# Performance work log

Measured on AMD Instinct MI355X. Metric: run time of the kernel, lower is better.

Reference implementation:

```python
import jax, jax.numpy as jnp
import numpy as np

B, C, H, W = 4, 256, 64, 64
C8 = C // 8


def setup_inputs() -> dict:
    key = jax.random.key(0)
    ks = jax.random.split(key, 9)
    s_in = 1.0 / np.sqrt(C)
    return {
        "x": jax.random.normal(ks[0], (B, C, H, W), dtype=jnp.float32),
        "Wq": jax.random.normal(ks[1], (C8, C), dtype=jnp.float32) * s_in,
        "bq": jax.random.normal(ks[2], (C8,), dtype=jnp.float32) * 0.01,
        "Wk": jax.random.normal(ks[3], (C8, C), dtype=jnp.float32) * s_in,
        "bk": jax.random.normal(ks[4], (C8,), dtype=jnp.float32) * 0.01,
        "Wv": jax.random.normal(ks[5], (C, C), dtype=jnp.float32) * s_in,
        "bv": jax.random.normal(ks[6], (C,), dtype=jnp.float32) * 0.01,
        "Wo": jax.random.normal(ks[7], (C, C), dtype=jnp.float32) * s_in,
        "bo": jax.random.normal(ks[8], (C,), dtype=jnp.float32) * 0.01,
    }


def reference(x, Wq, bq, Wk, bk, Wv, bv, Wo, bo):
    b, c, h, w = x.shape
    n = h * w
    xf = x.reshape(b, c, n)                                   # (B, C, N)
    # 1x1 convs are channel GEMMs
    q = jnp.einsum('bcn,dc->bnd', xf, Wq) + bq                # (B, N, C8)
    k = jnp.einsum('bcn,dc->bdn', xf, Wk) + bk[:, None]       # (B, C8, N)
    v = jnp.einsum('bcn,dc->bdn', xf, Wv) + bv[:, None]       # (B, C, N)
    energy = jnp.einsum('bnd,bdm->bnm', q, k)                 # (B, N, N)
    attn = jax.nn.softmax(energy, axis=-1)
    # out[b,c,i] = sum_j v[b,c,j] * attn[b,i,j]
    out = jnp.einsum('bcj,bij->bci', v, attn)                 # (B, C, N)
    out = out.reshape(b, c, h, w) + x                         # residual
    out = jnp.einsum('bchw,dc->bdhw', out, Wo) + bo[None, :, None, None]
    return out
```

## Files before the change

### kernel.cpp

```cpp
#include <hip/hip_runtime.h>

#define DEV __device__ __forceinline__

constexpr int B_  = 4;
constexpr int C_  = 256;
constexpr int C8_ = 32;
constexpr int N_  = 4096;

using u16 = unsigned short;
using u32 = unsigned int;

typedef __attribute__((ext_vector_type(8))) short bf16x8;
typedef __attribute__((ext_vector_type(4))) float f32x4;

DEV float bf2f(u16 u) { return __uint_as_float(((u32)u) << 16); }
DEV u16   f2bf(float f) {
  u32 i = __float_as_uint(f);
  i += 0x7fffu + ((i >> 16) & 1u);
  return (u16)(i >> 16);
}

DEV void cvt8(const float* p, bf16x8& hi, bf16x8& lo) {
  float4 a = *(const float4*)p;
  float4 b = *(const float4*)(p + 4);
  float f[8] = {a.x, a.y, a.z, a.w, b.x, b.y, b.z, b.w};
  #pragma unroll
  for (int j = 0; j < 8; ++j) {
    u16 h = f2bf(f[j]);
    hi[j] = (short)h;
    lo[j] = (short)f2bf(f[j] - bf2f(h));
  }
}

__global__ __launch_bounds__(256) void qkv_mfma(
    const float* __restrict__ x,
    const float* __restrict__ Wq, const float* __restrict__ bq,
    const float* __restrict__ Wk, const float* __restrict__ bk,
    const float* __restrict__ Wv, const float* __restrict__ bv,
    u16* __restrict__ qt, u16* __restrict__ kt, u16* __restrict__ vb,
    u16* __restrict__ xT)
{
  __shared__ __align__(16) u16 xh[64][264];
  __shared__ __align__(16) u16 xl[64][264];

  const int tid  = threadIdx.x;
  const int lane = tid & 63;
  const int w    = tid >> 6;
  const int m    = lane & 15;
  const int quad = lane >> 4;
  const int b    = blockIdx.y;
  const int n0   = blockIdx.x * 64;

  {
    const int nl = tid & 63, cb = tid >> 6;
    #pragma unroll 4
    for (int cc = 0; cc < 64; ++cc) {
      int c = cb + cc * 4;
      float v = x[((size_t)b * C_ + c) * N_ + n0 + nl];
      u16 h = f2bf(v);
      xh[nl][c] = h;
      xl[nl][c] = f2bf(v - bf2f(h));
    }
  }
  __syncthreads();

  #pragma unroll
  for (int it = 0; it < 8; ++it) {
    int idx = tid + it * 256;
    int n = idx >> 5, q = idx & 31;
    *(uint4*)&xT[((size_t)b * N_ + n0 + n) * C_ + q * 8] = *(const uint4*)&xh[n][q * 8];
  }

  f32x4 ov[4][4];
  f32x4 oq[4];
  #pragma unroll
  for (int dt = 0; dt < 4; ++dt)
    #pragma unroll
    for (int nt = 0; nt < 4; ++nt) ov[dt][nt] = (f32x4){0.f, 0.f, 0.f, 0.f};
  #pragma unroll
  for (int nt = 0; nt < 4; ++nt) oq[nt] = (f32x4){0.f, 0.f, 0.f, 0.f};

  const float* Wqk = (w < 2) ? (Wq + (size_t)(w * 16) * C_)
                             : (Wk + (size_t)((w - 2) * 16) * C_);

  for (int K = 0; K < 8; ++K) {
    bf16x8 xfh[4], xfl[4];
    #pragma unroll
    for (int nt = 0; nt < 4; ++nt) {
      xfh[nt] = *(const bf16x8*)&xh[nt * 16 + m][K * 32 + quad * 8];
      xfl[nt] = *(const bf16x8*)&xl[nt * 16 + m][K * 32 + quad * 8];
    }
    #pragma unroll
    for (int dt = 0; dt < 4; ++dt) {
      bf16x8 whi, wlo;
      cvt8(Wv + (size_t)(64 * w + dt * 16 + m) * C_ + K * 32 + quad * 8, whi, wlo);
      #pragma unroll
      for (int nt = 0; nt < 4; ++nt) {
        ov[dt][nt] = __builtin_amdgcn_mfma_f32_16x16x32_bf16(whi, xfh[nt], ov[dt][nt], 0, 0, 0);
        ov[dt][nt] = __builtin_amdgcn_mfma_f32_16x16x32_bf16(whi, xfl[nt], ov[dt][nt], 0, 0, 0);
        ov[dt][nt] = __builtin_amdgcn_mfma_f32_16x16x32_bf16(wlo, xfh[nt], ov[dt][nt], 0, 0, 0);
      }
    }
    {
      bf16x8 bhi, blo;
      cvt8(Wqk + (size_t)m * C_ + K * 32 + quad * 8, bhi, blo);
      #pragma unroll
      for (int nt = 0; nt < 4; ++nt) {
        oq[nt] = __builtin_amdgcn_mfma_f32_16x16x32_bf16(xfh[nt], bhi, oq[nt], 0, 0, 0);
        oq[nt] = __builtin_amdgcn_mfma_f32_16x16x32_bf16(xfl[nt], bhi, oq[nt], 0, 0, 0);
        oq[nt] = __builtin_amdgcn_mfma_f32_16x16x32_bf16(xfh[nt], blo, oq[nt], 0, 0, 0);
      }
    }
  }

  #pragma unroll
  for (int dt = 0; dt < 4; ++dt) {
    #pragma unroll
    for (int r = 0; r < 4; ++r) {
      int oc = 64 * w + dt * 16 + quad * 4 + r;
      float bias = bv[oc];
      #pragma unroll
      for (int nt = 0; nt < 4; ++nt)
        vb[((size_t)b * C_ + oc) * N_ + n0 + nt * 16 + m] = f2bf(ov[dt][nt][r] + bias);
    }
  }
  {
    u16* qk_out = (w < 2) ? qt : kt;
    const float* qk_bias = (w < 2) ? bq : bk;
    int dbase = (w & 1) * 16;
    float bias = qk_bias[dbase + m];
    #pragma unroll
    for (int nt = 0; nt < 4; ++nt)
      #pragma unroll
      for (int r = 0; r < 4; ++r)
        qk_out[((size_t)b * N_ + n0 + nt * 16 + quad * 4 + r) * C8_ + dbase + m] =
            f2bf(oq[nt][r] + bias);
  }
}

__global__ __launch_bounds__(256) void attn_mfma(
    const u16* __restrict__ qt,
    const u16* __restrict__ kt,
    const u16* __restrict__ vb,
    float* __restrict__ Opart,
    float* __restrict__ ml)
{
  __shared__ __align__(16) u16  ps[2][64][136];
  __shared__ __align__(16) float als[2][64];

  const int tid  = threadIdx.x;
  const int lane = tid & 63;
  const int w    = tid >> 6;
  const int m    = lane & 15;
  const int quad = lane >> 4;

  const int lid = blockIdx.x + gridDim.x * (blockIdx.y + gridDim.y * blockIdx.z);
  const int grp = lid & 7;
  const int ksl = grp & 1;
  const int b   = grp >> 1;
  const int i0  = (lid >> 3) * 64;

  const bf16x8 qfrag =
      *(const bf16x8*)(qt + ((size_t)b * N_ + i0 + w * 16 + m) * C8_ + quad * 8);

  const u16* kbase = kt + (size_t)b * N_ * C8_;
  const u16* vrow  = vb + ((size_t)b * C_ + w * 64 + m) * N_;

  f32x4 o[4][4];
  #pragma unroll
  for (int t = 0; t < 4; ++t)
    #pragma unroll
    for (int ct = 0; ct < 4; ++ct) o[t][ct] = (f32x4){0.f, 0.f, 0.f, 0.f};
  float m_r = -1e30f, l_r = 0.f;

  const int jbeg = ksl * 2048, jend = jbeg + 2048;
  int buf = 0;

  for (int j0 = jbeg; j0 < jend; j0 += 128, buf ^= 1) {
    bf16x8 kA[8];
    #pragma unroll
    for (int t = 0; t < 8; ++t)
      kA[t] = *(const bf16x8*)(kbase + (size_t)(j0 + t * 16 + m) * C8_ + quad * 8);
    bf16x8 vB[4][4];
    #pragma unroll
    for (int ct = 0; ct < 4; ++ct)
      #pragma unroll
      for (int kk = 0; kk < 4; ++kk)
        vB[ct][kk] = *(const bf16x8*)(vrow + (size_t)ct * 16 * N_ + j0 + kk * 32 + quad * 8);

    f32x4 s[8];
    #pragma unroll
    for (int t = 0; t < 8; ++t)
      s[t] = __builtin_amdgcn_mfma_f32_16x16x32_bf16(
          kA[t], qfrag, (f32x4){0.f, 0.f, 0.f, 0.f}, 0, 0, 0);

    float mx = -1e30f;
    #pragma unroll
    for (int t = 0; t < 8; ++t)
      #pragma unroll
      for (int r = 0; r < 4; ++r) mx = fmaxf(mx, s[t][r]);
    mx = fmaxf(mx, __shfl_xor(mx, 16));
    mx = fmaxf(mx, __shfl_xor(mx, 32));
    float mn = fmaxf(m_r, mx);
    float al = __expf(m_r - mn);
    m_r = mn;
    float p[8][4], sm = 0.f;
    #pragma unroll
    for (int t = 0; t < 8; ++t)
      #pragma unroll
      for (int r = 0; r < 4; ++r) {
        p[t][r] = __expf(s[t][r] - mn);
        sm += p[t][r];
      }
    sm += __shfl_xor(sm, 16);
    sm += __shfl_xor(sm, 32);
    l_r = l_r * al + sm;

    #pragma unroll
    for (int t = 0; t < 8; ++t) {
      u32 lo = (u32)f2bf(p[t][0]) | ((u32)f2bf(p[t][1]) << 16);
      u32 hi = (u32)f2bf(p[t][2]) | ((u32)f2bf(p[t][3]) << 16);
      *(uint2*)&ps[buf][w * 16 + m][t * 16 + quad * 4] = make_uint2(lo, hi);
    }
    if (quad == 0) als[buf][w * 16 + m] = al;

    __syncthreads();

    #pragma unroll
    for (int t = 0; t < 4; ++t) {
      float4 alv = *(const float4*)&als[buf][t * 16 + quad * 4];
      #pragma unroll
      for (int ct = 0; ct < 4; ++ct) {
        o[t][ct][0] *= alv.x; o[t][ct][1] *= alv.y;
        o[t][ct][2] *= alv.z; o[t][ct][3] *= alv.w;
      }
    }

    #pragma unroll
    for (int t = 0; t < 4; ++t) {
      #pragma unroll
      for (int kk = 0; kk < 4; ++kk) {
        bf16x8 pf = *(const bf16x8*)&ps[buf][t * 16 + m][kk * 32 + quad * 8];
        #pragma unroll
        for (int ct = 0; ct < 4; ++ct)
          o[t][ct] = __builtin_amdgcn_mfma_f32_16x16x32_bf16(pf, vB[ct][kk], o[t][ct], 0, 0, 0);
      }
    }
  }

  float* Ob = Opart + (size_t)ksl * B_ * N_ * C_ + ((size_t)b * N_ + i0) * C_ + w * 64;
  #pragma unroll
  for (int t = 0; t < 4; ++t)
    #pragma unroll
    for (int ct = 0; ct < 4; ++ct)
      #pragma unroll
      for (int r = 0; r < 4; ++r)
        Ob[(size_t)(t * 16 + quad * 4 + r) * C_ + ct * 16 + m] = o[t][ct][r];

  if (quad == 0) {
    size_t mli = ((size_t)ksl * B_ + b) * N_ + i0 + w * 16 + m;
    ml[mli] = m_r;
    ml[(size_t)2 * B_ * N_ + mli] = l_r;
  }
}

__global__ __launch_bounds__(256) void combine(
    const float* __restrict__ Opart, const float* __restrict__ ml,
    u16* __restrict__ hb)
{
  __shared__ __align__(16) u16 st[64][264];
  const int tid = threadIdx.x;
  const int b   = blockIdx.y;
  const int n0  = blockIdx.x * 64;
  const int nl  = tid & 63;
  const int cg  = tid >> 6;

  size_t base = (size_t)b * N_ + n0 + nl;
  float m0 = ml[base];
  float m1 = ml[(size_t)B_ * N_ + base];
  float l0 = ml[(size_t)2 * B_ * N_ + base];
  float l1 = ml[(size_t)3 * B_ * N_ + base];
  float M  = fmaxf(m0, m1);
  float w0 = __expf(m0 - M), w1 = __expf(m1 - M);
  float inv = 1.f / (l0 * w0 + l1 * w1);
  w0 *= inv; w1 *= inv;

  const float* O0 = Opart + base * C_ + cg * 64;
  const float* O1 = O0 + (size_t)B_ * N_ * C_;
  #pragma unroll
  for (int cc = 0; cc < 64; cc += 4) {
    float4 a  = *(const float4*)(O0 + cc);
    float4 c2 = *(const float4*)(O1 + cc);
    u32 lo = (u32)f2bf(a.x * w0 + c2.x * w1) | ((u32)f2bf(a.y * w0 + c2.y * w1) << 16);
    u32 hi = (u32)f2bf(a.z * w0 + c2.z * w1) | ((u32)f2bf(a.w * w0 + c2.w * w1) << 16);
    *(uint2*)&st[nl][cg * 64 + cc] = make_uint2(lo, hi);
  }
  __syncthreads();

  #pragma unroll
  for (int it = 0; it < 8; ++it) {
    int idx = tid + it * 256;
    int n = idx >> 5, q = idx & 31;
    *(uint4*)&hb[((size_t)b * N_ + n0 + n) * C_ + q * 8] = *(const uint4*)&st[n][q * 8];
  }
}

__global__ __launch_bounds__(256) void out_mfma(
    const u16* __restrict__ hb, const u16* __restrict__ xT,
    const float* __restrict__ Wo, const float* __restrict__ bo,
    float* __restrict__ out)
{
  const int tid  = threadIdx.x;
  const int lane = tid & 63;
  const int w    = tid >> 6;
  const int m    = lane & 15;
  const int quad = lane >> 4;
  const int b    = blockIdx.y;
  const int n0   = blockIdx.x * 64;

  f32x4 o[4][4];
  #pragma unroll
  for (int dt = 0; dt < 4; ++dt)
    #pragma unroll
    for (int nt = 0; nt < 4; ++nt) o[dt][nt] = (f32x4){0.f, 0.f, 0.f, 0.f};

  for (int K = 0; K < 8; ++K) {
    bf16x8 hf[4], xf[4];
    #pragma unroll
    for (int nt = 0; nt < 4; ++nt) {
      size_t row = (size_t)b * N_ + n0 + nt * 16 + m;
      hf[nt] = *(const bf16x8*)(hb + row * C_ + K * 32 + quad * 8);
      xf[nt] = *(const bf16x8*)(xT + row * C_ + K * 32 + quad * 8);
    }
    #pragma unroll
    for (int dt = 0; dt < 4; ++dt) {
      bf16x8 whi, wlo;
      cvt8(Wo + (size_t)(64 * w + dt * 16 + m) * C_ + K * 32 + quad * 8, whi, wlo);
      #pragma unroll
      for (int nt = 0; nt < 4; ++nt) {
        o[dt][nt] = __builtin_amdgcn_mfma_f32_16x16x32_bf16(whi, hf[nt], o[dt][nt], 0, 0, 0);
        o[dt][nt] = __builtin_amdgcn_mfma_f32_16x16x32_bf16(wlo, hf[nt], o[dt][nt], 0, 0, 0);
        o[dt][nt] = __builtin_amdgcn_mfma_f32_16x16x32_bf16(whi, xf[nt], o[dt][nt], 0, 0, 0);
        o[dt][nt] = __builtin_amdgcn_mfma_f32_16x16x32_bf16(wlo, xf[nt], o[dt][nt], 0, 0, 0);
      }
    }
  }

  #pragma unroll
  for (int dt = 0; dt < 4; ++dt)
    #pragma unroll
    for (int r = 0; r < 4; ++r) {
      int d = 64 * w + dt * 16 + quad * 4 + r;
      float bias = bo[d];
      #pragma unroll
      for (int nt = 0; nt < 4; ++nt)
        out[((size_t)b * C_ + d) * N_ + n0 + nt * 16 + m] = o[dt][nt][r] + bias;
    }
}

extern "C" void kernel_launch(void* const* d_in, const int* in_sizes, int n_in,
                              void* d_out, int out_size, void* d_ws, size_t ws_size,
                              hipStream_t stream)
{
  const float* x  = (const float*)d_in[0];
  const float* Wq = (const float*)d_in[1];
  const float* bq = (const float*)d_in[2];
  const float* Wk = (const float*)d_in[3];
  const float* bk = (const float*)d_in[4];
  const float* Wv = (const float*)d_in[5];
  const float* bv = (const float*)d_in[6];
  const float* Wo = (const float*)d_in[7];
  const float* bo = (const float*)d_in[8];

  u16* qt = (u16*)d_ws;
  u16* kt = qt + (size_t)B_ * N_ * C8_;
  u16* vb = kt + (size_t)B_ * N_ * C8_;
  u16* hb = vb + (size_t)B_ * C_ * N_;
  u16* xT = hb + (size_t)B_ * C_ * N_;
  float* Opart = (float*)(xT + (size_t)B_ * N_ * C_);
  float* ml = Opart + (size_t)2 * B_ * N_ * C_;

  float* out = (float*)d_out;

  qkv_mfma<<<dim3(N_ / 64, B_), 256, 0, stream>>>(
      x, Wq, bq, Wk, bk, Wv, bv, qt, kt, vb, xT);
  attn_mfma<<<dim3(N_ / 64, 2, B_), 256, 0, stream>>>(qt, kt, vb, Opart, ml);
  combine<<<dim3(N_ / 64, B_), 256, 0, stream>>>(Opart, ml, hb);
  out_mfma<<<dim3(N_ / 64, B_), 256, 0, stream>>>(hb, xT, Wo, bo, out);
}
```

Before: 228.7 us.

## Presplit weights, transpose x separately, prefetch K/V in attention, fuse combine into output GEMM

Adds a weight-split kernel that converts the weights to bf16 hi/lo pairs once, and an x-transpose kernel that writes hi/lo bf16 copies of x. The QKV and output GEMMs now read these directly with 32-wide tiles, which doubles the number of blocks. The attention kernel software-prefetches the next K and V fragments, keeps half of V resident, and skips rescaling when no row max changed. The separate combine kernel is folded into the output GEMM, which reads the fp32 partials directly. This removes redundant per-block conversion work and a launch, at the cost of extra kernels, more workspace traffic and higher register pressure.

```diff
diff --git a/kernel.cpp b/kernel.cpp
--- a/kernel.cpp
+++ b/kernel.cpp
@@ -20,117 +20,134 @@
   return (u16)(i >> 16);
 }
 
-DEV void cvt8(const float* p, bf16x8& hi, bf16x8& lo) {
-  float4 a = *(const float4*)p;
-  float4 b = *(const float4*)(p + 4);
-  float f[8] = {a.x, a.y, a.z, a.w, b.x, b.y, b.z, b.w};
-  #pragma unroll
-  for (int j = 0; j < 8; ++j) {
-    u16 h = f2bf(f[j]);
-    hi[j] = (short)h;
-    lo[j] = (short)f2bf(f[j] - bf2f(h));
+__global__ __launch_bounds__(256) void wsplit(
+    const float* __restrict__ Wq, const float* __restrict__ Wk,
+    const float* __restrict__ Wv, const float* __restrict__ Wo,
+    u16* __restrict__ WqH, u16* __restrict__ WqL,
+    u16* __restrict__ WkH, u16* __restrict__ WkL,
+    u16* __restrict__ WvH, u16* __restrict__ WvL,
+    u16* __restrict__ WoH, u16* __restrict__ WoL)
+{
+  int i = blockIdx.x * 256 + threadIdx.x;
+  const float* src; u16 *h, *l; int off;
+  if (i < 8192)        { src = Wq; h = WqH; l = WqL; off = i; }
+  else if (i < 16384)  { src = Wk; h = WkH; l = WkL; off = i - 8192; }
+  else if (i < 81920)  { src = Wv; h = WvH; l = WvL; off = i - 16384; }
+  else                 { src = Wo; h = WoH; l = WoL; off = i - 81920; }
+  float v = src[off];
+  u16 hi = f2bf(v);
+  h[off] = hi;
+  l[off] = f2bf(v - bf2f(hi));
+}
+
+__global__ __launch_bounds__(256) void xprep(
+    const float* __restrict__ x, u16* __restrict__ xTh, u16* __restrict__ xTl)
+{
+  __shared__ float tf[64][65];
+  const int tid = threadIdx.x;
+  const int b = blockIdx.z, c0 = blockIdx.y * 64, n0 = blockIdx.x * 64;
+  const int nl = tid & 63, cb = tid >> 6;
+
+  #pragma unroll
+  for (int cc = 0; cc < 16; ++cc) {
+    int cl = cb * 16 + cc;
+    tf[nl][cl] = x[((size_t)b * C_ + c0 + cl) * N_ + n0 + nl];
+  }
+  __syncthreads();
+
+  #pragma unroll
+  for (int it = 0; it < 2; ++it) {
+    int idx = tid + it * 256;
+    int n = idx >> 3, q = idx & 7;
+    u32 ph[4], pl[4];
+    #pragma unroll
+    for (int j = 0; j < 4; ++j) {
+      float v0 = tf[n][q * 8 + 2 * j], v1 = tf[n][q * 8 + 2 * j + 1];
+      u16 h0 = f2bf(v0), h1 = f2bf(v1);
+      ph[j] = (u32)h0 | ((u32)h1 << 16);
+      pl[j] = (u32)f2bf(v0 - bf2f(h0)) | ((u32)f2bf(v1 - bf2f(h1)) << 16);
+    }
+    size_t off = ((size_t)b * N_ + n0 + n) * C_ + c0 + q * 8;
+    *(uint4*)&xTh[off] = make_uint4(ph[0], ph[1], ph[2], ph[3]);
+    *(uint4*)&xTl[off] = make_uint4(pl[0], pl[1], pl[2], pl[3]);
   }
 }
 
 __global__ __launch_bounds__(256) void qkv_mfma(
-    const float* __restrict__ x,
-    const float* __restrict__ Wq, const float* __restrict__ bq,
-    const float* __restrict__ Wk, const float* __restrict__ bk,
-    const float* __restrict__ Wv, const float* __restrict__ bv,
-    u16* __restrict__ qt, u16* __restrict__ kt, u16* __restrict__ vb,
-    u16* __restrict__ xT)
-{
-  __shared__ __align__(16) u16 xh[64][264];
-  __shared__ __align__(16) u16 xl[64][264];
-
-  const int tid  = threadIdx.x;
-  const int lane = tid & 63;
-  const int w    = tid >> 6;
-  const int m    = lane & 15;
-  const int quad = lane >> 4;
-  const int b    = blockIdx.y;
-  const int n0   = blockIdx.x * 64;
-
-  {
-    const int nl = tid & 63, cb = tid >> 6;
-    #pragma unroll 4
-    for (int cc = 0; cc < 64; ++cc) {
-      int c = cb + cc * 4;
-      float v = x[((size_t)b * C_ + c) * N_ + n0 + nl];
-      u16 h = f2bf(v);
-      xh[nl][c] = h;
-      xl[nl][c] = f2bf(v - bf2f(h));
-    }
-  }
-  __syncthreads();
-
-  #pragma unroll
-  for (int it = 0; it < 8; ++it) {
-    int idx = tid + it * 256;
-    int n = idx >> 5, q = idx & 31;
-    *(uint4*)&xT[((size_t)b * N_ + n0 + n) * C_ + q * 8] = *(const uint4*)&xh[n][q * 8];
-  }
-
-  f32x4 ov[4][4];
-  f32x4 oq[4];
+    const u16* __restrict__ xTh, const u16* __restrict__ xTl,
+    const u16* __restrict__ WqH, const u16* __restrict__ WqL,
+    const u16* __restrict__ WkH, const u16* __restrict__ WkL,
+    const u16* __restrict__ WvH, const u16* __restrict__ WvL,
+    const float* __restrict__ bq, const float* __restrict__ bk,
+    const float* __restrict__ bv,
+    u16* __restrict__ qt, u16* __restrict__ kt, u16* __restrict__ vb)
+{
+  const int tid = threadIdx.x;
+  const int lane = tid & 63, w = tid >> 6, m = lane & 15, quad = lane >> 4;
+  const int b = blockIdx.y, n0 = blockIdx.x * 32;
+
+  const u16* qkH = (w < 2) ? (WqH + (size_t)(w * 16 + m) * C_)
+                           : (WkH + (size_t)((w - 2) * 16 + m) * C_);
+  const u16* qkL = (w < 2) ? (WqL + (size_t)(w * 16 + m) * C_)
+                           : (WkL + (size_t)((w - 2) * 16 + m) * C_);
+  const size_t nr0 = (size_t)b * N_ + n0 + m;
+
+  f32x4 ov[4][2], oq[2];
   #pragma unroll
   for (int dt = 0; dt < 4; ++dt)
     #pragma unroll
-    for (int nt = 0; nt < 4; ++nt) ov[dt][nt] = (f32x4){0.f, 0.f, 0.f, 0.f};
-  #pragma unroll
-  for (int nt = 0; nt < 4; ++nt) oq[nt] = (f32x4){0.f, 0.f, 0.f, 0.f};
-
-  const float* Wqk = (w < 2) ? (Wq + (size_t)(w * 16) * C_)
-                             : (Wk + (size_t)((w - 2) * 16) * C_);
+    for (int nt = 0; nt < 2; ++nt) ov[dt][nt] = (f32x4){0.f, 0.f, 0.f, 0.f};
+  #pragma unroll
+  for (int nt = 0; nt < 2; ++nt) oq[nt] = (f32x4){0.f, 0.f, 0.f, 0.f};
 
   for (int K = 0; K < 8; ++K) {
-    bf16x8 xfh[4], xfl[4];
-    #pragma unroll
-    for (int nt = 0; nt < 4; ++nt) {
-      xfh[nt] = *(const bf16x8*)&xh[nt * 16 + m][K * 32 + quad * 8];
-      xfl[nt] = *(const bf16x8*)&xl[nt * 16 + m][K * 32 + quad * 8];
+    const int ko = K * 32 + quad * 8;
+    bf16x8 xh[2], xl[2];
+    #pragma unroll
+    for (int nt = 0; nt < 2; ++nt) {
+      xh[nt] = *(const bf16x8*)(xTh + (nr0 + nt * 16) * C_ + ko);
+      xl[nt] = *(const bf16x8*)(xTl + (nr0 + nt * 16) * C_ + ko);
     }
     #pragma unroll
     for (int dt = 0; dt < 4; ++dt) {
-      bf16x8 whi, wlo;
-      cvt8(Wv + (size_t)(64 * w + dt * 16 + m) * C_ + K * 32 + quad * 8, whi, wlo);
-      #pragma unroll
-      for (int nt = 0; nt < 4; ++nt) {
-        ov[dt][nt] = __builtin_amdgcn_mfma_f32_16x16x32_bf16(whi, xfh[nt], ov[dt][nt], 0, 0, 0);
-        ov[dt][nt] = __builtin_amdgcn_mfma_f32_16x16x32_bf16(whi, xfl[nt], ov[dt][nt], 0, 0, 0);
-        ov[dt][nt] = __builtin_amdgcn_mfma_f32_16x16x32_bf16(wlo, xfh[nt], ov[dt][nt], 0, 0, 0);
+      bf16x8 whi = *(const bf16x8*)(WvH + (size_t)(64 * w + dt * 16 + m) * C_ + ko);
+      bf16x8 wlo = *(const bf16x8*)(WvL + (size_t)(64 * w + dt * 16 + m) * C_ + ko);
+      #pragma unroll
+      for (int nt = 0; nt < 2; ++nt) {
+        ov[dt][nt] = __builtin_amdgcn_mfma_f32_16x16x32_bf16(whi, xh[nt], ov[dt][nt], 0, 0, 0);
+        ov[dt][nt] = __builtin_amdgcn_mfma_f32_16x16x32_bf16(whi, xl[nt], ov[dt][nt], 0, 0, 0);
+        ov[dt][nt] = __builtin_amdgcn_mfma_f32_16x16x32_bf16(wlo, xh[nt], ov[dt][nt], 0, 0, 0);
       }
     }
     {
-      bf16x8 bhi, blo;
-      cvt8(Wqk + (size_t)m * C_ + K * 32 + quad * 8, bhi, blo);
-      #pragma unroll
-      for (int nt = 0; nt < 4; ++nt) {
-        oq[nt] = __builtin_amdgcn_mfma_f32_16x16x32_bf16(xfh[nt], bhi, oq[nt], 0, 0, 0);
-        oq[nt] = __builtin_amdgcn_mfma_f32_16x16x32_bf16(xfl[nt], bhi, oq[nt], 0, 0, 0);
-        oq[nt] = __builtin_amdgcn_mfma_f32_16x16x32_bf16(xfh[nt], blo, oq[nt], 0, 0, 0);
+      bf16x8 bhi = *(const bf16x8*)(qkH + ko);
+      bf16x8 blo = *(const bf16x8*)(qkL + ko);
+      #pragma unroll
+      for (int nt = 0; nt < 2; ++nt) {
+        oq[nt] = __builtin_amdgcn_mfma_f32_16x16x32_bf16(xh[nt], bhi, oq[nt], 0, 0, 0);
+        oq[nt] = __builtin_amdgcn_mfma_f32_16x16x32_bf16(xl[nt], bhi, oq[nt], 0, 0, 0);
+        oq[nt] = __builtin_amdgcn_mfma_f32_16x16x32_bf16(xh[nt], blo, oq[nt], 0, 0, 0);
       }
     }
   }
 
   #pragma unroll
-  for (int dt = 0; dt < 4; ++dt) {
+  for (int dt = 0; dt < 4; ++dt)
     #pragma unroll
     for (int r = 0; r < 4; ++r) {
       int oc = 64 * w + dt * 16 + quad * 4 + r;
       float bias = bv[oc];
       #pragma unroll
-      for (int nt = 0; nt < 4; ++nt)
+      for (int nt = 0; nt < 2; ++nt)
         vb[((size_t)b * C_ + oc) * N_ + n0 + nt * 16 + m] = f2bf(ov[dt][nt][r] + bias);
     }
-  }
   {
     u16* qk_out = (w < 2) ? qt : kt;
-    const float* qk_bias = (w < 2) ? bq : bk;
+    const float* qbias = (w < 2) ? bq : bk;
     int dbase = (w & 1) * 16;
-    float bias = qk_bias[dbase + m];
-    #pragma unroll
-    for (int nt = 0; nt < 4; ++nt)
+    float bias = qbias[dbase + m];
+    #pragma unroll
+    for (int nt = 0; nt < 2; ++nt)
       #pragma unroll
       for (int r = 0; r < 4; ++r)
         qk_out[((size_t)b * N_ + n0 + nt * 16 + quad * 4 + r) * C8_ + dbase + m] =
@@ -138,31 +155,23 @@
   }
 }
 
-__global__ __launch_bounds__(256) void attn_mfma(
-    const u16* __restrict__ qt,
-    const u16* __restrict__ kt,
+__global__ __launch_bounds__(256, 2) void attn_mfma(
+    const u16* __restrict__ qt, const u16* __restrict__ kt,
     const u16* __restrict__ vb,
-    float* __restrict__ Opart,
-    float* __restrict__ ml)
+    float* __restrict__ Opart, float* __restrict__ ml)
 {
   __shared__ __align__(16) u16  ps[2][64][136];
   __shared__ __align__(16) float als[2][64];
 
-  const int tid  = threadIdx.x;
-  const int lane = tid & 63;
-  const int w    = tid >> 6;
-  const int m    = lane & 15;
-  const int quad = lane >> 4;
+  const int tid = threadIdx.x, lane = tid & 63, w = tid >> 6;
+  const int m = lane & 15, quad = lane >> 4;
 
   const int lid = blockIdx.x + gridDim.x * (blockIdx.y + gridDim.y * blockIdx.z);
-  const int grp = lid & 7;
-  const int ksl = grp & 1;
-  const int b   = grp >> 1;
-  const int i0  = (lid >> 3) * 64;
+  const int grp = lid & 7, ksl = grp & 1, b = grp >> 1;
+  const int i0 = (lid >> 3) * 64;
 
   const bf16x8 qfrag =
       *(const bf16x8*)(qt + ((size_t)b * N_ + i0 + w * 16 + m) * C8_ + quad * 8);
-
   const u16* kbase = kt + (size_t)b * N_ * C8_;
   const u16* vrow  = vb + ((size_t)b * C_ + w * 64 + m) * N_;
 
@@ -176,17 +185,22 @@
   const int jbeg = ksl * 2048, jend = jbeg + 2048;
   int buf = 0;
 
+  bf16x8 kA[8], vB01[2][4], vB23[2][4];
+  #pragma unroll
+  for (int t = 0; t < 8; ++t)
+    kA[t] = *(const bf16x8*)(kbase + (size_t)(jbeg + t * 16 + m) * C8_ + quad * 8);
+  #pragma unroll
+  for (int ct = 0; ct < 2; ++ct)
+    #pragma unroll
+    for (int kk = 0; kk < 4; ++kk)
+      vB01[ct][kk] = *(const bf16x8*)(vrow + (size_t)ct * 16 * N_ + jbeg + kk * 32 + quad * 8);
+
   for (int j0 = jbeg; j0 < jend; j0 += 128, buf ^= 1) {
-    bf16x8 kA[8];
-    #pragma unroll
-    for (int t = 0; t < 8; ++t)
-      kA[t] = *(const bf16x8*)(kbase + (size_t)(j0 + t * 16 + m) * C8_ + quad * 8);
-    bf16x8 vB[4][4];
-    #pragma unroll
-    for (int ct = 0; ct < 4; ++ct)
+    #pragma unroll
+    for (int ct = 0; ct < 2; ++ct)
       #pragma unroll
       for (int kk = 0; kk < 4; ++kk)
-        vB[ct][kk] = *(const bf16x8*)(vrow + (size_t)ct * 16 * N_ + j0 + kk * 32 + quad * 8);
+        vB23[ct][kk] = *(const bf16x8*)(vrow + (size_t)(ct + 2) * 16 * N_ + j0 + kk * 32 + quad * 8);
 
     f32x4 s[8];
     #pragma unroll
@@ -226,14 +240,34 @@
 
     __syncthreads();
 
-    #pragma unroll
-    for (int t = 0; t < 4; ++t) {
-      float4 alv = *(const float4*)&als[buf][t * 16 + quad * 4];
-      #pragma unroll
-      for (int ct = 0; ct < 4; ++ct) {
-        o[t][ct][0] *= alv.x; o[t][ct][1] *= alv.y;
-        o[t][ct][2] *= alv.z; o[t][ct][3] *= alv.w;
-      }
+    const int jn = j0 + 128;
+    bf16x8 kAn[8], vBn[2][4];
+    if (jn < jend) {
+      #pragma unroll
+      for (int t = 0; t < 8; ++t)
+        kAn[t] = *(const bf16x8*)(kbase + (size_t)(jn + t * 16 + m) * C8_ + quad * 8);
+      #pragma unroll
+      for (int ct = 0; ct < 2; ++ct)
+        #pragma unroll
+        for (int kk = 0; kk < 4; ++kk)
+          vBn[ct][kk] = *(const bf16x8*)(vrow + (size_t)ct * 16 * N_ + jn + kk * 32 + quad * 8);
+    }
+
+    float4 alv[4];
+    #pragma unroll
+    for (int t = 0; t < 4; ++t) alv[t] = *(const float4*)&als[buf][t * 16 + quad * 4];
+    float am = 1.f;
+    #pragma unroll
+    for (int t = 0; t < 4; ++t)
+      am = fminf(am, fminf(fminf(alv[t].x, alv[t].y), fminf(alv[t].z, alv[t].w)));
+    if (__any(am < 1.f)) {
+      #pragma unroll
+      for (int t = 0; t < 4; ++t)
+        #pragma unroll
+        for (int ct = 0; ct < 4; ++ct) {
+          o[t][ct][0] *= alv[t].x; o[t][ct][1] *= alv[t].y;
+          o[t][ct][2] *= alv[t].z; o[t][ct][3] *= alv[t].w;
+        }
     }
 
     #pragma unroll
@@ -241,10 +275,20 @@
       #pragma unroll
       for (int kk = 0; kk < 4; ++kk) {
         bf16x8 pf = *(const bf16x8*)&ps[buf][t * 16 + m][kk * 32 + quad * 8];
+        o[t][0] = __builtin_amdgcn_mfma_f32_16x16x32_bf16(pf, vB01[0][kk], o[t][0], 0, 0, 0);
+        o[t][1] = __builtin_amdgcn_mfma_f32_16x16x32_bf16(pf, vB01[1][kk], o[t][1], 0, 0, 0);
+        o[t][2] = __builtin_amdgcn_mfma_f32_16x16x32_bf16(pf, vB23[0][kk], o[t][2], 0, 0, 0);
+        o[t][3] = __builtin_amdgcn_mfma_f32_16x16x32_bf16(pf, vB23[1][kk], o[t][3], 0, 0, 0);
+      }
+    }
+
+    if (jn < jend) {
+      #pragma unroll
+      for (int t = 0; t < 8; ++t) kA[t] = kAn[t];
+      #pragma unroll
+      for (int ct = 0; ct < 2; ++ct)
         #pragma unroll
-        for (int ct = 0; ct < 4; ++ct)
-          o[t][ct] = __builtin_amdgcn_mfma_f32_16x16x32_bf16(pf, vB[ct][kk], o[t][ct], 0, 0, 0);
-      }
+        for (int kk = 0; kk < 4; ++kk) vB01[ct][kk] = vBn[ct][kk];
     }
   }
 
@@ -264,80 +308,64 @@
   }
 }
 
-__global__ __launch_bounds__(256) void combine(
+__global__ __launch_bounds__(256) void out_mfma(
     const float* __restrict__ Opart, const float* __restrict__ ml,
-    u16* __restrict__ hb)
-{
-  __shared__ __align__(16) u16 st[64][264];
+    const u16* __restrict__ xTh,
+    const u16* __restrict__ WoH, const u16* __restrict__ WoL,
+    const float* __restrict__ bo, float* __restrict__ out)
+{
   const int tid = threadIdx.x;
-  const int b   = blockIdx.y;
-  const int n0  = blockIdx.x * 64;
-  const int nl  = tid & 63;
-  const int cg  = tid >> 6;
-
-  size_t base = (size_t)b * N_ + n0 + nl;
-  float m0 = ml[base];
-  float m1 = ml[(size_t)B_ * N_ + base];
-  float l0 = ml[(size_t)2 * B_ * N_ + base];
-  float l1 = ml[(size_t)3 * B_ * N_ + base];
-  float M  = fmaxf(m0, m1);
-  float w0 = __expf(m0 - M), w1 = __expf(m1 - M);
-  float inv = 1.f / (l0 * w0 + l1 * w1);
-  w0 *= inv; w1 *= inv;
-
-  const float* O0 = Opart + base * C_ + cg * 64;
-  const float* O1 = O0 + (size_t)B_ * N_ * C_;
-  #pragma unroll
-  for (int cc = 0; cc < 64; cc += 4) {
-    float4 a  = *(const float4*)(O0 + cc);
-    float4 c2 = *(const float4*)(O1 + cc);
-    u32 lo = (u32)f2bf(a.x * w0 + c2.x * w1) | ((u32)f2bf(a.y * w0 + c2.y * w1) << 16);
-    u32 hi = (u32)f2bf(a.z * w0 + c2.z * w1) | ((u32)f2bf(a.w * w0 + c2.w * w1) << 16);
-    *(uint2*)&st[nl][cg * 64 + cc] = make_uint2(lo, hi);
-  }
-  __syncthreads();
-
-  #pragma unroll
-  for (int it = 0; it < 8; ++it) {
-    int idx = tid + it * 256;
-    int n = idx >> 5, q = idx & 31;
-    *(uint4*)&hb[((size_t)b * N_ + n0 + n) * C_ + q * 8] = *(const uint4*)&st[n][q * 8];
-  }
-}
-
-__global__ __launch_bounds__(256) void out_mfma(
-    const u16* __restrict__ hb, const u16* __restrict__ xT,
-    const float* __restrict__ Wo, const float* __restrict__ bo,
-    float* __restrict__ out)
-{
-  const int tid  = threadIdx.x;
-  const int lane = tid & 63;
-  const int w    = tid >> 6;
-  const int m    = lane & 15;
-  const int quad = lane >> 4;
-  const int b    = blockIdx.y;
-  const int n0   = blockIdx.x * 64;
-
-  f32x4 o[4][4];
+  const int lane = tid & 63, w = tid >> 6, m = lane & 15, quad = lane >> 4;
+  const int b = blockIdx.y, n0 = blockIdx.x * 32;
+  constexpr size_t BN = (size_t)B_ * N_;
+
+  float w0[2], w1[2];
+  size_t nrow[2];
+  #pragma unroll
+  for (int nt = 0; nt < 2; ++nt) {
+    nrow[nt] = (size_t)b * N_ + n0 + nt * 16 + m;
+    float m0 = ml[nrow[nt]], m1 = ml[BN + nrow[nt]];
+    float l0 = ml[2 * BN + nrow[nt]], l1 = ml[3 * BN + nrow[nt]];
+    float M = fmaxf(m0, m1);
+    float a0 = __expf(m0 - M), a1 = __expf(m1 - M);
+    float inv = 1.f / (l0 * a0 + l1 * a1);
+    w0[nt] = a0 * inv; w1[nt] = a1 * inv;
+  }
+
+  f32x4 o[4][2];
   #pragma unroll
   for (int dt = 0; dt < 4; ++dt)
     #pragma unroll
-    for (int nt = 0; nt < 4; ++nt) o[dt][nt] = (f32x4){0.f, 0.f, 0.f, 0.f};
+    for (int nt = 0; nt < 2; ++nt) o[dt][nt] = (f32x4){0.f, 0.f, 0.f, 0.f};
 
   for (int K = 0; K < 8; ++K) {
-    bf16x8 hf[4], xf[4];
-    #pragma unroll
-    for (int nt = 0; nt < 4; ++nt) {
-      size_t row = (size_t)b * N_ + n0 + nt * 16 + m;
-      hf[nt] = *(const bf16x8*)(hb + row * C_ + K * 32 + quad * 8);
-      xf[nt] = *(const bf16x8*)(xT + row * C_ + K * 32 + quad * 8);
+    const int ko = K * 32 + quad * 8;
+    bf16x8 hf[2], xf[2];
+    #pragma unroll
+    for (int nt = 0; nt < 2; ++nt) {
+      const float* O0 = Opart + nrow[nt] * C_ + ko;
+      const float* O1 = O0 + BN * C_;
+      float4 a = *(const float4*)O0,  a2 = *(const float4*)(O0 + 4);
+      float4 c = *(const float4*)O1,  c2 = *(const float4*)(O1 + 4);
+      float hv[8] = {
+        a.x * w0[nt] + c.x * w1[nt],  a.y * w0[nt] + c.y * w1[nt],
+        a.z * w0[nt] + c.z * w1[nt],  a.w * w0[nt] + c.w * w1[nt],
+        a2.x * w0[nt] + c2.x * w1[nt], a2.y * w0[nt] + c2.y * w1[nt],
+        a2.z * w0[nt] + c2.z * w1[nt], a2.w * w0[nt] + c2.w * w1[nt] };
+      uint4 pk;
+      pk.x = (u32)f2bf(hv[0]) | ((u32)f2bf(hv[1]) << 16);
+      pk.y = (u32)f2bf(hv[2]) | ((u32)f2bf(hv[3]) << 16);
+      pk.z = (u32)f2bf(hv[4]) | ((u32)f2bf(hv[5]) << 16);
+      pk.w = (u32)f2bf(hv[6]) | ((u32)f2bf(hv[7]) << 16);
+      hf[nt] = *(const bf16x8*)&pk;
+      xf[nt] = *(const bf16x8*)(xTh + nrow[nt] * C_ + ko);
     }
     #pragma unroll
     for (int dt = 0; dt < 4; ++dt) {
-      bf16x8 whi, wlo;
-      cvt8(Wo + (size_t)(64 * w + dt * 16 + m) * C_ + K * 32 + quad * 8, whi, wlo);
-      #pragma unroll
-      for (int nt = 0; nt < 4; ++nt) {
+      bf16x8 whi = *(const bf16x8*)(WoH + (size_t)(64 * w + dt * 16 + m) * C_ + ko);
+      bf16x8 wlo = *(const bf16x8*)(WoL + (size_t)(64 * w + dt * 16 + m) * C_ + ko);
+      #pragma unroll
+      for (int nt = 0; nt < 2; ++nt) {
         o[dt][nt] = __builtin_amdgcn_mfma_f32_16x16x32_bf16(whi, hf[nt], o[dt][nt], 0, 0, 0);
         o[dt][nt] = __builtin_amdgcn_mfma_f32_16x16x32_bf16(wlo, hf[nt], o[dt][nt], 0, 0, 0);
         o[dt][nt] = __builtin_amdgcn_mfma_f32_16x16x32_bf16(whi, xf[nt], o[dt][nt], 0, 0, 0);
@@ -353,7 +381,7 @@
       int d = 64 * w + dt * 16 + quad * 4 + r;
       float bias = bo[d];
       #pragma unroll
-      for (int nt = 0; nt < 4; ++nt)
+      for (int nt = 0; nt < 2; ++nt)
         out[((size_t)b * C_ + d) * N_ + n0 + nt * 16 + m] = o[dt][nt][r] + bias;
     }
 }
@@ -372,19 +400,30 @@
   const float* Wo = (const float*)d_in[7];
   const float* bo = (const float*)d_in[8];
 
-  u16* qt = (u16*)d_ws;
-  u16* kt = qt + (size_t)B_ * N_ * C8_;
-  u16* vb = kt + (size_t)B_ * N_ * C8_;
-  u16* hb = vb + (size_t)B_ * C_ * N_;
-  u16* xT = hb + (size_t)B_ * C_ * N_;
-  float* Opart = (float*)(xT + (size_t)B_ * N_ * C_);
+  u16* p = (u16*)d_ws;
+  u16* qt  = p;  p += (size_t)B_ * N_ * C8_;
+  u16* kt  = p;  p += (size_t)B_ * N_ * C8_;
+  u16* vb  = p;  p += (size_t)B_ * C_ * N_;
+  u16* xTh = p;  p += (size_t)B_ * N_ * C_;
+  u16* xTl = p;  p += (size_t)B_ * N_ * C_;
+  u16* WqH = p;  p += 8192;
+  u16* WqL = p;  p += 8192;
+  u16* WkH = p;  p += 8192;
+  u16* WkL = p;  p += 8192;
+  u16* WvH = p;  p += 65536;
+  u16* WvL = p;  p += 65536;
+  u16* WoH = p;  p += 65536;
+  u16* WoL = p;  p += 65536;
+  float* Opart = (float*)p;
   float* ml = Opart + (size_t)2 * B_ * N_ * C_;
 
   float* out = (float*)d_out;
 
-  qkv_mfma<<<dim3(N_ / 64, B_), 256, 0, stream>>>(
-      x, Wq, bq, Wk, bk, Wv, bv, qt, kt, vb, xT);
+  wsplit<<<576, 256, 0, stream>>>(Wq, Wk, Wv, Wo,
+      WqH, WqL, WkH, WkL, WvH, WvL, WoH, WoL);
+  xprep<<<dim3(N_ / 64, C_ / 64, B_), 256, 0, stream>>>(x, xTh, xTl);
+  qkv_mfma<<<dim3(N_ / 32, B_), 256, 0, stream>>>(
+      xTh, xTl, WqH, WqL, WkH, WkL, WvH, WvL, bq, bk, bv, qt, kt, vb);
   attn_mfma<<<dim3(N_ / 64, 2, B_), 256, 0, stream>>>(qt, kt, vb, Opart, ml);
-  combine<<<dim3(N_ / 64, B_), 256, 0, stream>>>(Opart, ml, hb);
-  out_mfma<<<dim3(N_ / 64, B_), 256, 0, stream>>>(hb, xT, Wo, bo, out);
-}
+  out_mfma<<<dim3(N_ / 32, B_), 256, 0, stream>>>(Opart, ml, xTh, WoH, WoL, bo, out);
+}
```

Measured after the change: 259.2 us. +13.4%, slower.
